# Kernel tuning notes

Measured on AMD Instinct MI355X. Metric: run time of the kernel, lower is better.

## Reference

```python
import jax, jax.numpy as jnp
import numpy as np

D_MODEL = 128
K_RED = 3          # fd_redundancy_k
MAX_ITERS = 16     # upper bound on the data-dependent while-loop; masked no-ops after convergence
NEG = -1e9


def setup_inputs() -> dict:
    key = jax.random.key(0)
    ks = jax.random.split(key, 10)
    B, U, S, D, F = 16, 2048, 512, D_MODEL, 32
    return {
        "user_enc": jax.random.normal(ks[0], (B, U, D), jnp.float32),
        "server_enc": jax.random.normal(ks[1], (B, S, D), jnp.float32),
        "users": jax.random.uniform(ks[2], (B, U, 6), jnp.float32),
        "servers": jax.random.uniform(ks[3], (B, S, 7), jnp.float32),
        "connect": jax.random.randint(ks[4], (B, U, S), 0, 2, jnp.int32),
        "fd_onehot": jax.random.randint(ks[5], (B, S, F), 0, 2, jnp.int32),
        "state_proj_w": jax.random.normal(ks[6], (D, 4), jnp.float32) * 0.05,
        "state_proj_b": jnp.zeros((D,), jnp.float32),
        "fd_bias": jnp.asarray(1.0, jnp.float32),
        "ptr_q_w": jax.random.normal(ks[7], (D, D), jnp.float32) * (D ** -0.5),
        "ptr_k_w": jax.random.normal(ks[8], (D, D), jnp.float32) * (D ** -0.5),
        "user_state_w": jax.random.normal(ks[9], (1, 3), jnp.float32) * 0.05,
        "score_bias": jnp.zeros((1,), jnp.float32),
    }


def _forward(user_enc, server_enc, users, servers, connect, fd_onehot,
             state_proj_w, state_proj_b, fd_bias, ptr_q_w, ptr_k_w,
             user_state_w, score_bias):
    B, U, _ = users.shape
    S = servers.shape[1]
    D = user_enc.shape[-1]
    needs = users[..., 2:6]                    # [B,U,4]
    init_cap = servers[..., 3:7]               # [B,S,4]
    connect_mask = connect.astype(bool)
    fd = fd_onehot.astype(jnp.float32)         # [B,S,F] in {0,1}
    F = fd.shape[-1]
    inv_sqrt_d = D ** -0.5
    tk = jnp.float32(max(K_RED, 1))
    q = user_enc @ ptr_q_w.T                   # [B,U,D]  (loop-invariant)
    u_ids = jnp.arange(U)
    s_ids = jnp.arange(S)

    def body(carry, _):
        alloc, cap, seen, logp, flag = carry
        replica_count = alloc.sum(-1)                                    # [B,U]
        need_more = replica_count < K_RED
        can_fulfill = jnp.all(cap[:, None] >= needs[:, :, None], axis=-1)  # [B,U,S]
        eligible = connect_mask & can_fulfill & need_more[..., None] & ~alloc
        go = flag & jnp.any(need_more) & jnp.any(eligible)

        # pointer-attention logits with dynamic server state
        is_new_fd = (jnp.einsum('buf,bsf->bus', seen, fd) < 0.5).astype(jnp.float32)
        cap_ratio = cap / jnp.maximum(init_cap, 1e-6)
        k_vec = (server_enc + cap_ratio @ state_proj_w.T + state_proj_b) @ ptr_k_w.T
        logits = jnp.einsum('bud,bsd->bus', q, k_vec) * inv_sqrt_d + score_bias
        logits = logits + fd_bias * is_new_fd
        rc = replica_count.astype(jnp.float32)
        user_state = jnp.stack([rc / tk,
                                jnp.clip(K_RED - rc, 0.0, None) / tk,
                                (replica_count == K_RED - 1).astype(jnp.float32)], axis=-1)
        logits = logits + user_state @ user_state_w.T                    # broadcast [B,U,1]

        cand = jnp.where(eligible, logits, NEG)
        # each valid server greedily proposes its best eligible user
        valid_server = jnp.any(eligible, axis=1)                         # [B,S]
        prop_u = jnp.argmax(cand, axis=1)                                # [B,S]
        prop_mask = valid_server[:, None, :] & (u_ids[None, :, None] == prop_u[:, None, :])
        logp_prop = jnp.max(cand, axis=1) - jax.nn.logsumexp(cand, axis=1)  # [B,S]

        # each proposed user accepts the highest-scoring proposing server
        acc_cand = jnp.where(prop_mask, logits, NEG)
        has_prop = jnp.any(prop_mask, axis=2)                            # [B,U]
        chosen_s = jnp.argmax(acc_cand, axis=2)                          # [B,U]
        accepted = has_prop[..., None] & (s_ids == chosen_s[..., None])  # [B,U,S]

        alloc = alloc | (accepted & go)
        fd_gain = (jnp.einsum('bus,bsf->buf', prop_mask.astype(jnp.float32), fd) > 0).astype(jnp.float32)
        seen = jnp.where(go, jnp.maximum(seen, fd_gain), seen)
        used = jnp.einsum('bus,buc->bsc', accepted.astype(jnp.float32), needs)
        cap = jnp.where(go, jnp.maximum(cap - used, 0.0), cap)
        gathered = jnp.take_along_axis(logp_prop, chosen_s, axis=1)      # [B,U]
        logp = logp + jnp.where(go & has_prop, gathered, 0.0)
        return (alloc, cap, seen, logp, go), None

    init = (jnp.zeros((B, U, S), bool), init_cap,
            jnp.zeros((B, U, F), jnp.float32), jnp.zeros((B, U), jnp.float32),
            jnp.asarray(True))
    (alloc, cap, seen, logp, _), _ = jax.lax.scan(body, init, None, length=MAX_ITERS)
    return logp.sum(axis=1), alloc, cap


def reference(user_enc, server_enc, users, servers, connect, fd_onehot,
              state_proj_w, state_proj_b, fd_bias, ptr_q_w, ptr_k_w,
              user_state_w, score_bias):
    # policy='greedy' branch of the original forward
    return _forward(user_enc, server_enc, users, servers, connect, fd_onehot,
                    state_proj_w, state_proj_b, fd_bias, ptr_q_w, ptr_k_w,
                    user_state_w, score_bias)
```

## Files before the change

### kernel.cpp

```cpp
#include <hip/hip_runtime.h>
#include <hip/hip_bf16.h>

#define B_N 16
#define U_N 2048
#define S_N 512
#define D_N 128
#define INV_SQRT_D 0.08838834764831845f

typedef unsigned long long ull;
typedef __attribute__((ext_vector_type(8))) short bf16x8;
typedef __attribute__((ext_vector_type(4))) float f32x4;
typedef __attribute__((ext_vector_type(4))) _Float16 f16x4;

__device__ __forceinline__ unsigned monof(float v) {
    unsigned b = __float_as_uint(v);
    return (b & 0x80000000u) ? ~b : (b | 0x80000000u);
}
__device__ __forceinline__ float unmonof(unsigned m) {
    unsigned b = (m & 0x80000000u) ? (m & 0x7fffffffu) : ~m;
    return __uint_as_float(b);
}
__device__ __forceinline__ unsigned short f2bf(float x) {
    unsigned u = __float_as_uint(x);
    return (unsigned short)((u + 0x7fffu + ((u >> 16) & 1u)) >> 16);
}

__global__ void init_state(const float* __restrict__ servers, const float* __restrict__ users,
                           const int* __restrict__ fd_onehot,
                           unsigned* allocU, uint4* alloc3, unsigned* rcArr, unsigned* seenArr,
                           float* logp, float* capA, float* invA, unsigned* fdm, float* nds,
                           unsigned* any_valid) {
    int i = blockIdx.x * 256 + threadIdx.x;
    if (i < B_N * U_N * 16) allocU[i] = 0u;
    if (i < B_N * U_N) {
        rcArr[i] = 0u; seenArr[i] = 0u; logp[i] = 0.f;
        alloc3[i] = make_uint4(0xFFFFFFFFu, 0xFFFFFFFFu, 0xFFFFFFFFu, 0xFFFFFFFFu);
        const float* up = users + (size_t)i * 6;
        nds[i * 4 + 0] = up[2]; nds[i * 4 + 1] = up[3];
        nds[i * 4 + 2] = up[4]; nds[i * 4 + 3] = up[5];
    }
    if (i < B_N * S_N) {
        const float* sp = servers + (size_t)i * 7;
        float4 c = make_float4(sp[3], sp[4], sp[5], sp[6]);
        ((float4*)capA)[i] = c;
        ((float4*)invA)[i] = make_float4(1.f / fmaxf(c.x, 1e-6f), 1.f / fmaxf(c.y, 1e-6f),
                                         1.f / fmaxf(c.z, 1e-6f), 1.f / fmaxf(c.w, 1e-6f));
        unsigned w = 0u;
        const int* fp = fd_onehot + (size_t)i * 32;
        #pragma unroll
        for (int f = 0; f < 32; ++f) w |= (fp[f] != 0 ? 1u : 0u) << f;
        fdm[i] = w;
    }
    if (i < 16) any_valid[i] = 0u;
}

__global__ void pack_connect(const int* __restrict__ connect, ull* __restrict__ connU) {
    int i = blockIdx.x * 4 + (threadIdx.x >> 6);
    int lane = threadIdx.x & 63;
    const int* row = connect + (size_t)i * S_N;
    #pragma unroll
    for (int c = 0; c < 8; ++c) {
        ull m = __ballot(row[c * 64 + lane] != 0);
        if (lane == 0) connU[(size_t)i * 8 + c] = m;
    }
}

template <bool ABIAS, int OUTMODE>
__global__ __launch_bounds__(256) void gemm_nt(const float* __restrict__ A, const float* __restrict__ Bm,
                                               const float* __restrict__ abias, float* __restrict__ C,
                                               unsigned short* __restrict__ C16,
                                               int M, int N, int K, float scale) {
    __shared__ float As[16][68];
    __shared__ float Bs[16][68];
    int z = blockIdx.z;
    const float* Ab = A + (size_t)z * M * K;
    const float* Bb = Bm;
    int m0 = blockIdx.x * 64, n0 = blockIdx.y * 64;
    int tid = threadIdx.x;
    int tx = tid & 15, ty = tid >> 4;
    int lrow = tid >> 2, lk = (tid & 3) * 4;
    float acc[4][4] = {};
    for (int k0 = 0; k0 < K; k0 += 16) {
        float4 av = *(const float4*)(Ab + (size_t)(m0 + lrow) * K + k0 + lk);
        float4 bv = *(const float4*)(Bb + (size_t)(n0 + lrow) * K + k0 + lk);
        if (ABIAS) {
            av.x += abias[k0 + lk]; av.y += abias[k0 + lk + 1];
            av.z += abias[k0 + lk + 2]; av.w += abias[k0 + lk + 3];
        }
        __syncthreads();
        As[lk + 0][lrow] = av.x; As[lk + 1][lrow] = av.y; As[lk + 2][lrow] = av.z; As[lk + 3][lrow] = av.w;
        Bs[lk + 0][lrow] = bv.x; Bs[lk + 1][lrow] = bv.y; Bs[lk + 2][lrow] = bv.z; Bs[lk + 3][lrow] = bv.w;
        __syncthreads();
        #pragma unroll
        for (int kk = 0; kk < 16; ++kk) {
            float4 a = *(const float4*)&As[kk][ty * 4];
            float4 bq = *(const float4*)&Bs[kk][tx * 4];
            float ar[4] = {a.x, a.y, a.z, a.w}, br[4] = {bq.x, bq.y, bq.z, bq.w};
            #pragma unroll
            for (int ii = 0; ii < 4; ++ii)
                #pragma unroll
                for (int jj = 0; jj < 4; ++jj) acc[ii][jj] += ar[ii] * br[jj];
        }
    }
    #pragma unroll
    for (int ii = 0; ii < 4; ++ii) {
        float4 o = make_float4(acc[ii][0] * scale, acc[ii][1] * scale,
                               acc[ii][2] * scale, acc[ii][3] * scale);
        size_t idx = (size_t)z * M * N + (size_t)(m0 + ty * 4 + ii) * N + n0 + tx * 4;
        if (OUTMODE != 1) *(float4*)(C + idx) = o;
        if (OUTMODE != 0) {
            ushort4 ob;
            ob.x = f2bf(o.x); ob.y = f2bf(o.y); ob.z = f2bf(o.z); ob.w = f2bf(o.w);
            *(ushort4*)(C16 + idx) = ob;
        }
    }
}

__global__ void m3_kernel(const float* __restrict__ kw, const float* __restrict__ spw,
                          const float* __restrict__ qw, float* __restrict__ M3) {
    __shared__ float M2s[512];
    int t = threadIdx.x;
    {
        int d = t >> 2, c = t & 3;
        float acc = 0.f;
        for (int e = 0; e < 128; ++e) acc += kw[d * 128 + e] * spw[e * 4 + c];
        M2s[d * 4 + c] = acc * INV_SQRT_D;
    }
    __syncthreads();
    {
        int e = t >> 2, c = t & 3;
        float acc = 0.f;
        for (int d = 0; d < 128; ++d) acc += qw[d * 128 + e] * M2s[d * 4 + c];
        M3[e * 4 + c] = acc;
    }
}

__global__ void qm_kernel(const float* __restrict__ enc, const float* __restrict__ M3, float* __restrict__ qm) {
    __shared__ float qs[64][129];
    __shared__ float m3s[512];
    int b = blockIdx.y, u0 = blockIdx.x * 64;
    int t = threadIdx.x;
    for (int i = t; i < 512; i += 256) m3s[i] = M3[i];
    #pragma unroll
    for (int it = 0; it < 8; ++it) {
        int f4 = t + 256 * it;
        int row = f4 >> 5;
        int col = (f4 & 31) * 4;
        float4 v = *(const float4*)(enc + ((size_t)(b * U_N + u0 + row)) * D_N + col);
        qs[row][col] = v.x; qs[row][col + 1] = v.y; qs[row][col + 2] = v.z; qs[row][col + 3] = v.w;
    }
    __syncthreads();
    int ul = t >> 2, c = t & 3;
    float acc = 0.f;
    for (int d = 0; d < 128; ++d) acc += qs[ul][d] * m3s[d * 4 + c];
    qm[((size_t)(b * U_N + u0 + ul)) * 4 + c] = acc;
}

__global__ __launch_bounds__(256) void qk_mfma(const unsigned short* __restrict__ qb,
                                               const unsigned short* __restrict__ kb,
                                               _Float16* __restrict__ qkh) {
    const int b = blockIdx.z, u0 = blockIdx.x * 128, s0 = blockIdx.y * 64;
    const int t = threadIdx.x, w = t >> 6, l = t & 63;
    const int lr = l & 15, lq = l >> 4;
    const unsigned short* Ab = qb + ((size_t)(b * U_N + u0 + w * 32 + lr)) * D_N + lq * 8;
    const unsigned short* Bb = kb + ((size_t)(b * S_N + s0 + lr)) * D_N + lq * 8;
    f32x4 acc[2][4] = {};
    #pragma unroll
    for (int kt = 0; kt < 4; ++kt) {
        bf16x8 a0 = *(const bf16x8*)(Ab + kt * 32);
        bf16x8 a1 = *(const bf16x8*)(Ab + 16 * D_N + kt * 32);
        #pragma unroll
        for (int c = 0; c < 4; ++c) {
            bf16x8 bf = *(const bf16x8*)(Bb + c * 16 * D_N + kt * 32);
            acc[0][c] = __builtin_amdgcn_mfma_f32_16x16x32_bf16(a0, bf, acc[0][c], 0, 0, 0);
            acc[1][c] = __builtin_amdgcn_mfma_f32_16x16x32_bf16(a1, bf, acc[1][c], 0, 0, 0);
        }
    }
    __shared__ _Float16 Cs[128][72];
    #pragma unroll
    for (int mt = 0; mt < 2; ++mt)
        #pragma unroll
        for (int c = 0; c < 4; ++c)
            #pragma unroll
            for (int r = 0; r < 4; ++r)
                Cs[w * 32 + mt * 16 + lq * 4 + r][c * 16 + lr] = (_Float16)acc[mt][c][r];
    __syncthreads();
    #pragma unroll
    for (int k = 0; k < 4; ++k) {
        int row = (t >> 3) + k * 32;
        int sg = (t & 7) * 8;
        uint4 v = *(const uint4*)&Cs[row][sg];
        *(uint4*)(qkh + ((size_t)(b * U_N + u0 + row)) * S_N + s0 + sg) = v;
    }
}

__global__ __launch_bounds__(1024, 1) void iter_score(
    const _Float16* __restrict__ qkh, const float* __restrict__ qm4,
    const float* __restrict__ nds, const unsigned* __restrict__ connU32,
    const uint4* __restrict__ alloc3, const unsigned* __restrict__ rcArr,
    const unsigned* __restrict__ seenArr, const unsigned* __restrict__ fdm_,
    const float* __restrict__ capA, const float* __restrict__ invA,
    const float* __restrict__ usw, const float* __restrict__ sbp, const float* __restrict__ fdbp,
    ull* __restrict__ keypart, float* __restrict__ sumpart,
    const unsigned* __restrict__ any_valid, int iter) {
    if (iter > 0 && any_valid[iter - 1] == 0u) return;
    const int tid = threadIdx.x;
    const int b = blockIdx.x & 15;
    const int ublk = blockIdx.x >> 4;
    const int u0 = ublk << 7;
    const int h = tid >> 7;
    const int sl = tid & 127;
    const int s0 = sl * 4;
    const float w0 = usw[0], w1 = usw[1], w2 = usw[2], sb = sbp[0], fdb = fdbp[0];
    const float ub0 = sb + w1;
    const float ub1 = sb + w0 * (1.f / 3.f) + w1 * (2.f / 3.f);
    const float ub2 = sb + w0 * (2.f / 3.f) + w1 * (1.f / 3.f) + w2;
    const int bsb = b * S_N + s0;
    float4 cap[4], cr[4]; unsigned fq[4];
    #pragma unroll
    for (int j = 0; j < 4; ++j) {
        cap[j] = ((const float4*)capA)[bsb + j];
        float4 iv = ((const float4*)invA)[bsb + j];
        cr[j] = make_float4(cap[j].x * iv.x, cap[j].y * iv.y, cap[j].z * iv.z, cap[j].w * iv.w);
        fq[j] = fdm_[bsb + j];
    }
    ull k[4] = {0ULL, 0ULL, 0ULL, 0ULL};
    float e[4] = {0.f, 0.f, 0.f, 0.f};
    const int gub = b * U_N + u0 + h * 16;
    const _Float16* qkbase = qkh + ((size_t)gub) * S_N + s0;
    const int cwbase = gub * 16 + (sl >> 3);
    const int nsh = (sl & 7) * 4;
    #pragma unroll 2
    for (int uu = 0; uu < 16; ++uu) {
        const int gu = gub + uu;
        const unsigned rcu = rcArr[gu];
        if (rcu < 3u) {
            const f16x4 qv = *(const f16x4*)(qkbase + (size_t)uu * S_N);
            const float4 qmv = ((const float4*)qm4)[gu];
            const float4 ndv = ((const float4*)nds)[gu];
            const unsigned snu = seenArr[gu];
            const uint4 al = alloc3[gu];
            const unsigned nib = connU32[cwbase + uu * 16] >> nsh;
            const float add = (rcu == 0u) ? ub0 : ((rcu == 1u) ? ub1 : ub2);
            const unsigned uinv = ~(unsigned)(u0 + h * 16 + uu);
            #pragma unroll
            for (int j = 0; j < 4; ++j) {
                const unsigned us = (unsigned)(s0 + j);
                const bool ful = (cap[j].x >= ndv.x) & (cap[j].y >= ndv.y) &
                                 (cap[j].z >= ndv.z) & (cap[j].w >= ndv.w);
                const bool aok = (al.x != us) & (al.y != us) & (al.z != us);
                const bool el = (((nib >> j) & 1u) != 0u) & ful & aok;
                const float lg = (float)qv[j] + qmv.x * cr[j].x + qmv.y * cr[j].y +
                                 qmv.z * cr[j].z + qmv.w * cr[j].w + add +
                                 (((snu & fq[j]) == 0u) ? fdb : 0.f);
                if (el) {
                    const ull kk = ((ull)monof(lg) << 32) | uinv;
                    k[j] = k[j] > kk ? k[j] : kk;
                    e[j] += __expf(lg);
                }
            }
        }
    }
    __shared__ ull mk[8][128][4];
    __shared__ float me[8][128][4];
    #pragma unroll
    for (int j = 0; j < 4; ++j) { mk[h][sl][j] = k[j]; me[h][sl][j] = e[j]; }
    __syncthreads();
    if (tid < 512) {
        const int sl2 = tid >> 2, j2 = tid & 3;
        ull kb2 = mk[0][sl2][j2];
        float eb = me[0][sl2][j2];
        #pragma unroll
        for (int o = 1; o < 8; ++o) {
            const ull kk = mk[o][sl2][j2];
            kb2 = kk > kb2 ? kk : kb2;
            eb += me[o][sl2][j2];
        }
        const size_t p = (size_t)ublk * (B_N * S_N) + (size_t)b * S_N + sl2 * 4 + j2;
        keypart[p] = kb2;
        sumpart[p] = eb;
    }
}

__global__ __launch_bounds__(1024) void iter_midapply(
    const ull* __restrict__ keypart, const float* __restrict__ sumpart,
    const unsigned* __restrict__ fdm_, const float* __restrict__ nds,
    uint4* __restrict__ alloc3, unsigned* __restrict__ allocU,
    unsigned* __restrict__ rcArr, unsigned* __restrict__ seenArr,
    float* __restrict__ capA, float* __restrict__ logp,
    unsigned* __restrict__ any_valid, int iter) {
    if (iter > 0 && any_valid[iter - 1] == 0u) return;
    __shared__ ull ukeyL[2048];
    __shared__ unsigned sgL[2048];
    __shared__ ull bkL[512];
    __shared__ float bsL[512];
    __shared__ float lpL[512];
    const int b = blockIdx.x, t = threadIdx.x;
    ukeyL[t] = 0ULL; ukeyL[t + 1024] = 0ULL;
    sgL[t] = 0u; sgL[t + 1024] = 0u;
    __syncthreads();
    const int s = t & 511, h = t >> 9;
    const int base = b * S_N + s;
    ull best = 0ULL; float ssum = 0.f;
    #pragma unroll
    for (int j = h * 8; j < h * 8 + 8; ++j) {
        const ull kk = keypart[(size_t)j * (B_N * S_N) + base];
        best = kk > best ? kk : best;
        ssum += sumpart[(size_t)j * (B_N * S_N) + base];
    }
    if (h == 0) { bkL[s] = best; bsL[s] = ssum; }
    __syncthreads();
    unsigned prop = 0u;
    if (h == 1) {
        const ull ob = bkL[s];
        best = ob > best ? ob : best;
        ssum += bsL[s];
        if (best != 0ULL) {
            const float mx = unmonof((unsigned)(best >> 32));
            const unsigned pu = ~(unsigned)best;
            lpL[s] = mx - __logf(ssum);
            const ull pk = ((ull)monof(mx) << 32) | (~(unsigned)s);
            atomicMax(&ukeyL[pu], pk);
            atomicOr(&sgL[pu], fdm_[base]);
            prop = 1u;
        }
    }
    const ull bal = __ballot(prop != 0u);
    if (bal != 0ULL && (t & 63) == 0) atomicOr(&any_valid[iter], 1u);
    __syncthreads();
    #pragma unroll
    for (int g = 0; g < 2; ++g) {
        const int u = t + g * 1024;
        const ull key = ukeyL[u];
        if (key != 0ULL) {
            const int gu = b * U_N + u;
            const unsigned s2 = ~(unsigned)key;
            const int bs2 = b * S_N + (int)s2;
            uint4 al = alloc3[gu];
            const unsigned r = rcArr[gu];
            if (r == 0u) al.x = s2; else if (r == 1u) al.y = s2; else al.z = s2;
            alloc3[gu] = al;
            allocU[gu * 16 + (s2 >> 5)] |= 1u << (s2 & 31u);
            const float4 nd = ((const float4*)nds)[gu];
            float4 cv = ((float4*)capA)[bs2];
            cv.x = fmaxf(cv.x - nd.x, 0.f); cv.y = fmaxf(cv.y - nd.y, 0.f);
            cv.z = fmaxf(cv.z - nd.z, 0.f); cv.w = fmaxf(cv.w - nd.w, 0.f);
            ((float4*)capA)[bs2] = cv;
            rcArr[gu] = r + 1u;
            logp[gu] += lpL[s2];
            seenArr[gu] |= sgL[u];
        }
    }
}

__global__ void finalize_logp(const float* __restrict__ logp, float* __restrict__ out) {
    int b = blockIdx.x, t = threadIdx.x;
    float s = 0.f;
    for (int u = t; u < U_N; u += 256) s += logp[b * U_N + u];
    #pragma unroll
    for (int m = 1; m < 64; m <<= 1) s += __shfl_xor(s, m, 64);
    __shared__ float r[4];
    if ((t & 63) == 0) r[t >> 6] = s;
    __syncthreads();
    if (t == 0) out[b] = r[0] + r[1] + r[2] + r[3];
}

__global__ void finalize_alloc(const unsigned* __restrict__ allocU, float* __restrict__ out) {
    int idx = blockIdx.x * 256 + threadIdx.x;
    int bu = idx >> 7;
    int s4 = (idx & 127) * 4;
    unsigned w = allocU[bu * 16 + (s4 >> 5)];
    float4 o;
    o.x = ((w >> ((s4 + 0) & 31)) & 1u) ? 1.f : 0.f;
    o.y = ((w >> ((s4 + 1) & 31)) & 1u) ? 1.f : 0.f;
    o.z = ((w >> ((s4 + 2) & 31)) & 1u) ? 1.f : 0.f;
    o.w = ((w >> ((s4 + 3) & 31)) & 1u) ? 1.f : 0.f;
    *(float4*)(out + 16 + (size_t)bu * S_N + s4) = o;
}

__global__ void finalize_cap(const float* __restrict__ capA, float* __restrict__ out) {
    int i = blockIdx.x * 256 + threadIdx.x;
    if (i < B_N * S_N * 4) out[16 + (size_t)B_N * U_N * S_N + i] = capA[i];
}

extern "C" void kernel_launch(void* const* d_in, const int* in_sizes, int n_in,
                              void* d_out, int out_size, void* d_ws, size_t ws_size,
                              hipStream_t stream) {
    const float* user_enc = (const float*)d_in[0];
    const float* server_enc = (const float*)d_in[1];
    const float* users = (const float*)d_in[2];
    const float* servers = (const float*)d_in[3];
    const int* connect = (const int*)d_in[4];
    const int* fd_onehot = (const int*)d_in[5];
    const float* state_proj_w = (const float*)d_in[6];
    const float* state_proj_b = (const float*)d_in[7];
    const float* fd_bias = (const float*)d_in[8];
    const float* ptr_q_w = (const float*)d_in[9];
    const float* ptr_k_w = (const float*)d_in[10];
    const float* user_state_w = (const float*)d_in[11];
    const float* score_bias = (const float*)d_in[12];
    float* out = (float*)d_out;

    char* w = (char*)d_ws;
    _Float16* qkh = (_Float16*)(w + 0);
    unsigned short* qb = (unsigned short*)(w + 33554432);
    unsigned short* kb = (unsigned short*)(w + 41943040);
    ull* keypart = (ull*)(w + 44040192);
    float* sumpart = (float*)(w + 45088768);
    float* qm = (float*)(w + 45613056);
    ull* connU = (ull*)(w + 46137344);
    unsigned* allocU = (unsigned*)(w + 48234496);
    uint4* alloc3 = (uint4*)(w + 50331648);
    float* nds = (float*)(w + 50855936);
    unsigned* fdm = (unsigned*)(w + 51380224);
    float* capA = (float*)(w + 51412992);
    float* invA = (float*)(w + 51544064);
    unsigned* rcArr = (unsigned*)(w + 51675136);
    unsigned* seenArr = (unsigned*)(w + 51806208);
    float* logp = (float*)(w + 51937280);
    float* M3 = (float*)(w + 52068352);
    unsigned* any_valid = (unsigned*)(w + 52070400);

    init_state<<<2048, 256, 0, stream>>>(servers, users, fd_onehot, allocU, alloc3, rcArr,
                                         seenArr, logp, capA, invA, fdm, nds, any_valid);
    pack_connect<<<8192, 256, 0, stream>>>(connect, connU);
    gemm_nt<true, 1><<<dim3(8, 2, 16), 256, 0, stream>>>(server_enc, ptr_k_w, state_proj_b,
                                                         nullptr, kb, S_N, D_N, D_N, INV_SQRT_D);
    gemm_nt<false, 1><<<dim3(32, 2, 16), 256, 0, stream>>>(user_enc, ptr_q_w, nullptr,
                                                           nullptr, qb, U_N, D_N, D_N, 1.0f);
    m3_kernel<<<1, 512, 0, stream>>>(ptr_k_w, state_proj_w, ptr_q_w, M3);
    qm_kernel<<<dim3(32, 16), 256, 0, stream>>>(user_enc, M3, qm);
    qk_mfma<<<dim3(16, 8, 16), 256, 0, stream>>>(qb, kb, qkh);
    for (int it = 0; it < 16; ++it) {
        iter_score<<<256, 1024, 0, stream>>>(qkh, qm, nds, (const unsigned*)connU, alloc3, rcArr,
                                             seenArr, fdm, capA, invA, user_state_w, score_bias,
                                             fd_bias, keypart, sumpart, any_valid, it);
        iter_midapply<<<16, 1024, 0, stream>>>(keypart, sumpart, fdm, nds, alloc3, allocU,
                                               rcArr, seenArr, capA, logp, any_valid, it);
    }
    finalize_logp<<<16, 256, 0, stream>>>(logp, out);
    finalize_alloc<<<16384, 256, 0, stream>>>(allocU, out);
    finalize_cap<<<128, 256, 0, stream>>>(capA, out);
}
```

Before: 463.4 us.

## Fuse iterative allocation loop into one cooperative kernel with grid syncs

New measurement: 936.0 us. 102% more time.

```diff
diff --git a/kernel.cpp b/kernel.cpp
--- a/kernel.cpp
+++ b/kernel.cpp
@@ -1,5 +1,8 @@
 #include <hip/hip_runtime.h>
 #include <hip/hip_bf16.h>
+#include <hip/hip_cooperative_groups.h>
+
+namespace cg = cooperative_groups;
 
 #define B_N 16
 #define U_N 2048
@@ -191,6 +194,209 @@
         int sg = (t & 7) * 8;
         uint4 v = *(const uint4*)&Cs[row][sg];
         *(uint4*)(qkh + ((size_t)(b * U_N + u0 + row)) * S_N + s0 + sg) = v;
+    }
+}
+
+__global__ __launch_bounds__(1024) void alloc_loop(
+    const _Float16* __restrict__ qkh, const float* __restrict__ qm4,
+    const float* __restrict__ nds, const unsigned* __restrict__ connU32,
+    uint4* __restrict__ alloc3, unsigned* __restrict__ allocU,
+    unsigned* __restrict__ rcArr, unsigned* __restrict__ seenArr,
+    const unsigned* __restrict__ fdm_,
+    float* __restrict__ capA, const float* __restrict__ invA,
+    const float* __restrict__ usw, const float* __restrict__ sbp,
+    const float* __restrict__ fdbp,
+    ull* __restrict__ keypart, float* __restrict__ sumpart,
+    float* __restrict__ logp, unsigned* __restrict__ any_valid,
+    float* __restrict__ out) {
+    cg::grid_group grid = cg::this_grid();
+    __shared__ __align__(16) char smem[49152];
+    ull (*mk)[128][4] = (ull (*)[128][4])smem;
+    float (*me)[128][4] = (float (*)[128][4])(smem + 32768);
+    ull* ukeyL = (ull*)smem;
+    unsigned* sgL = (unsigned*)(smem + 16384);
+    ull* bkL = (ull*)(smem + 24576);
+    float* bsL = (float*)(smem + 28672);
+    float* lpL = (float*)(smem + 30720);
+
+    const int tid = threadIdx.x;
+    const int b = blockIdx.x & 15;
+    const int ublk = blockIdx.x >> 4;
+    const int u0 = ublk << 7;
+    const int h = tid >> 7;
+    const int sl = tid & 127;
+    const int s0 = sl * 4;
+    const float w0 = usw[0], w1 = usw[1], w2 = usw[2], sb = sbp[0], fdb = fdbp[0];
+    const float ub0 = sb + w1;
+    const float ub1 = sb + w0 * (1.f / 3.f) + w1 * (2.f / 3.f);
+    const float ub2 = sb + w0 * (2.f / 3.f) + w1 * (1.f / 3.f) + w2;
+    const int bsb = b * S_N + s0;
+    const int gub = b * U_N + u0 + h * 16;
+    const _Float16* qkbase = qkh + (size_t)gub * S_N + s0;
+    const int cwbase = gub * 16 + (sl >> 3);
+    const int nsh = (sl & 7) * 4;
+    float4 iv[4]; unsigned fq[4];
+    #pragma unroll
+    for (int j = 0; j < 4; ++j) {
+        iv[j] = ((const float4*)invA)[bsb + j];
+        fq[j] = fdm_[bsb + j];
+    }
+    ull connbits = 0ULL;
+    #pragma unroll
+    for (int uu = 0; uu < 16; ++uu)
+        connbits |= (ull)((connU32[cwbase + uu * 16] >> nsh) & 0xFu) << (4 * uu);
+
+    for (int iter = 0; iter < 16; ++iter) {
+        float4 cap[4], cr[4];
+        #pragma unroll
+        for (int j = 0; j < 4; ++j) {
+            cap[j] = ((const float4*)capA)[bsb + j];
+            cr[j] = make_float4(cap[j].x * iv[j].x, cap[j].y * iv[j].y,
+                                cap[j].z * iv[j].z, cap[j].w * iv[j].w);
+        }
+        ull k[4] = {0ULL, 0ULL, 0ULL, 0ULL};
+        float e[4] = {0.f, 0.f, 0.f, 0.f};
+        #pragma unroll 2
+        for (int uu = 0; uu < 16; ++uu) {
+            const int gu = gub + uu;
+            const unsigned rcu = rcArr[gu];
+            if (rcu < 3u) {
+                const f16x4 qv = *(const f16x4*)(qkbase + (size_t)uu * S_N);
+                const float4 qmv = ((const float4*)qm4)[gu];
+                const float4 ndv = ((const float4*)nds)[gu];
+                const unsigned snu = seenArr[gu];
+                const uint4 al = alloc3[gu];
+                const unsigned nib = (unsigned)(connbits >> (4 * uu)) & 0xFu;
+                const float add = (rcu == 0u) ? ub0 : ((rcu == 1u) ? ub1 : ub2);
+                const unsigned uinv = ~(unsigned)(u0 + h * 16 + uu);
+                #pragma unroll
+                for (int j = 0; j < 4; ++j) {
+                    const unsigned us = (unsigned)(s0 + j);
+                    const bool ful = (cap[j].x >= ndv.x) & (cap[j].y >= ndv.y) &
+                                     (cap[j].z >= ndv.z) & (cap[j].w >= ndv.w);
+                    const bool aok = (al.x != us) & (al.y != us) & (al.z != us);
+                    const bool el = (((nib >> j) & 1u) != 0u) & ful & aok;
+                    const float lg = (float)qv[j] + qmv.x * cr[j].x + qmv.y * cr[j].y +
+                                     qmv.z * cr[j].z + qmv.w * cr[j].w + add +
+                                     (((snu & fq[j]) == 0u) ? fdb : 0.f);
+                    if (el) {
+                        const ull kk = ((ull)monof(lg) << 32) | uinv;
+                        k[j] = k[j] > kk ? k[j] : kk;
+                        e[j] += __expf(lg);
+                    }
+                }
+            }
+        }
+        #pragma unroll
+        for (int j = 0; j < 4; ++j) { mk[h][sl][j] = k[j]; me[h][sl][j] = e[j]; }
+        __syncthreads();
+        if (tid < 512) {
+            const int sl2 = tid >> 2, j2 = tid & 3;
+            ull kb2 = mk[0][sl2][j2];
+            float eb = me[0][sl2][j2];
+            #pragma unroll
+            for (int o = 1; o < 8; ++o) {
+                const ull kk = mk[o][sl2][j2];
+                kb2 = kk > kb2 ? kk : kb2;
+                eb += me[o][sl2][j2];
+            }
+            const size_t p = (size_t)ublk * (B_N * S_N) + (size_t)b * S_N + sl2 * 4 + j2;
+            keypart[p] = kb2;
+            sumpart[p] = eb;
+        }
+        grid.sync();
+        if (ublk == 0) {
+            ukeyL[tid] = 0ULL; ukeyL[tid + 1024] = 0ULL;
+            sgL[tid] = 0u; sgL[tid + 1024] = 0u;
+            __syncthreads();
+            const int s = tid & 511, hh = tid >> 9;
+            const int base = b * S_N + s;
+            ull best = 0ULL; float ssum = 0.f;
+            #pragma unroll
+            for (int j = hh * 8; j < hh * 8 + 8; ++j) {
+                const ull kk = keypart[(size_t)j * (B_N * S_N) + base];
+                best = kk > best ? kk : best;
+                ssum += sumpart[(size_t)j * (B_N * S_N) + base];
+            }
+            if (hh == 0) { bkL[s] = best; bsL[s] = ssum; }
+            __syncthreads();
+            unsigned prop = 0u;
+            if (hh == 1) {
+                const ull ob = bkL[s];
+                best = ob > best ? ob : best;
+                ssum += bsL[s];
+                if (best != 0ULL) {
+                    const float mx = unmonof((unsigned)(best >> 32));
+                    const unsigned pu = ~(unsigned)best;
+                    lpL[s] = mx - __logf(ssum);
+                    const ull pk = ((ull)monof(mx) << 32) | (~(unsigned)s);
+                    atomicMax(&ukeyL[pu], pk);
+                    atomicOr(&sgL[pu], fdm_[base]);
+                    prop = 1u;
+                }
+            }
+            const ull bal = __ballot(prop != 0u);
+            if (bal != 0ULL && (tid & 63) == 0) atomicOr(&any_valid[iter], 1u);
+            __syncthreads();
+            #pragma unroll
+            for (int g = 0; g < 2; ++g) {
+                const int u = tid + g * 1024;
+                const ull key = ukeyL[u];
+                if (key != 0ULL) {
+                    const int gu = b * U_N + u;
+                    const unsigned s2 = ~(unsigned)key;
+                    const int bs2 = b * S_N + (int)s2;
+                    uint4 al = alloc3[gu];
+                    const unsigned r = rcArr[gu];
+                    if (r == 0u) al.x = s2; else if (r == 1u) al.y = s2; else al.z = s2;
+                    alloc3[gu] = al;
+                    allocU[gu * 16 + (s2 >> 5)] |= 1u << (s2 & 31u);
+                    const float4 nd = ((const float4*)nds)[gu];
+                    float4 cv = ((float4*)capA)[bs2];
+                    cv.x = fmaxf(cv.x - nd.x, 0.f); cv.y = fmaxf(cv.y - nd.y, 0.f);
+                    cv.z = fmaxf(cv.z - nd.z, 0.f); cv.w = fmaxf(cv.w - nd.w, 0.f);
+                    ((float4*)capA)[bs2] = cv;
+                    rcArr[gu] = r + 1u;
+                    logp[gu] += lpL[s2];
+                    seenArr[gu] |= sgL[u];
+                }
+            }
+        }
+        grid.sync();
+        if (__hip_atomic_load(any_valid + iter, __ATOMIC_RELAXED,
+                              __HIP_MEMORY_SCOPE_AGENT) == 0u) break;
+    }
+    if (ublk == 0) {
+        float s = 0.f;
+        for (int u = tid; u < U_N; u += 1024) s += logp[b * U_N + u];
+        #pragma unroll
+        for (int m = 1; m < 64; m <<= 1) s += __shfl_xor(s, m, 64);
+        float* rr = (float*)smem;
+        if ((tid & 63) == 0) rr[tid >> 6] = s;
+        __syncthreads();
+        if (tid == 0) {
+            float tt = 0.f;
+            #pragma unroll
+            for (int i2 = 0; i2 < 16; ++i2) tt += rr[i2];
+            out[b] = tt;
+        }
+    }
+    if (ublk == 1) {
+        for (int i2 = tid; i2 < S_N * 4; i2 += 1024)
+            out[16 + (size_t)B_N * U_N * S_N + b * S_N * 4 + i2] = capA[b * S_N * 4 + i2];
+    }
+    {
+        const int rowbase = b * U_N + u0;
+        for (int i2 = tid; i2 < 128 * 128; i2 += 1024) {
+            const int row = i2 >> 7, s4 = (i2 & 127) * 4;
+            const unsigned wv = allocU[(rowbase + row) * 16 + (s4 >> 5)];
+            float4 o;
+            o.x = ((wv >> ((s4 + 0) & 31)) & 1u) ? 1.f : 0.f;
+            o.y = ((wv >> ((s4 + 1) & 31)) & 1u) ? 1.f : 0.f;
+            o.z = ((wv >> ((s4 + 2) & 31)) & 1u) ? 1.f : 0.f;
+            o.w = ((wv >> ((s4 + 3) & 31)) & 1u) ? 1.f : 0.f;
+            *(float4*)(out + 16 + (size_t)(rowbase + row) * S_N + s4) = o;
+        }
     }
 }
 
@@ -431,14 +637,28 @@
     m3_kernel<<<1, 512, 0, stream>>>(ptr_k_w, state_proj_w, ptr_q_w, M3);
     qm_kernel<<<dim3(32, 16), 256, 0, stream>>>(user_enc, M3, qm);
     qk_mfma<<<dim3(16, 8, 16), 256, 0, stream>>>(qb, kb, qkh);
-    for (int it = 0; it < 16; ++it) {
-        iter_score<<<256, 1024, 0, stream>>>(qkh, qm, nds, (const unsigned*)connU, alloc3, rcArr,
-                                             seenArr, fdm, capA, invA, user_state_w, score_bias,
-                                             fd_bias, keypart, sumpart, any_valid, it);
-        iter_midapply<<<16, 1024, 0, stream>>>(keypart, sumpart, fdm, nds, alloc3, allocU,
-                                               rcArr, seenArr, capA, logp, any_valid, it);
-    }
-    finalize_logp<<<16, 256, 0, stream>>>(logp, out);
-    finalize_alloc<<<16384, 256, 0, stream>>>(allocU, out);
-    finalize_cap<<<128, 256, 0, stream>>>(capA, out);
-}
+
+    const unsigned* connU32c = (const unsigned*)connU;
+    void* args[] = {(void*)&qkh, (void*)&qm, (void*)&nds, (void*)&connU32c,
+                    (void*)&alloc3, (void*)&allocU, (void*)&rcArr, (void*)&seenArr,
+                    (void*)&fdm, (void*)&capA, (void*)&invA,
+                    (void*)&user_state_w, (void*)&score_bias, (void*)&fd_bias,
+                    (void*)&keypart, (void*)&sumpart, (void*)&logp, (void*)&any_valid,
+                    (void*)&out};
+    hipError_t cerr = hipLaunchCooperativeKernel((const void*)alloc_loop, dim3(256), dim3(1024),
+                                                 args, 0, stream);
+    if (cerr != hipSuccess) {
+        (void)hipGetLastError();
+        for (int it = 0; it < 16; ++it) {
+            iter_score<<<256, 1024, 0, stream>>>(qkh, qm, nds, (const unsigned*)connU, alloc3,
+                                                 rcArr, seenArr, fdm, capA, invA, user_state_w,
+                                                 score_bias, fd_bias, keypart, sumpart,
+                                                 any_valid, it);
+            iter_midapply<<<16, 1024, 0, stream>>>(keypart, sumpart, fdm, nds, alloc3, allocU,
+                                                   rcArr, seenArr, capA, logp, any_valid, it);
+        }
+        finalize_logp<<<16, 256, 0, stream>>>(logp, out);
+        finalize_alloc<<<16384, 256, 0, stream>>>(allocU, out);
+        finalize_cap<<<128, 256, 0, stream>>>(capA, out);
+    }
+}
```
